# Optimization experiments

Hardware: AMD Instinct MI355X
Metric: run time of the kernel (lower is better)

Reference implementation:

```python
import jax, jax.numpy as jnp
import numpy as np

EPS_NORM = 1e-12   # F.normalize eps
EPS_DIST = 1e-4    # sqrt stabilizer from original code
EPSILON = 1e-8     # log stabilizer (forward default arg)


def setup_inputs() -> dict:
    key = jax.random.key(0)
    thought_vectors = jax.random.normal(key, (4, 2048, 1024), dtype=jnp.float32)
    return {"thought_vectors": thought_vectors}


def reference(thought_vectors):
    # NOTE: original code casts to fp32 then discards it by re-reshaping the
    # raw input; inputs here are already fp32 so the math is identical.
    D = thought_vectors.shape[-1]
    x = thought_vectors.reshape(-1, D)                          # [N, D]
    norm = jnp.linalg.norm(x, axis=-1, keepdims=True)
    x = x / jnp.maximum(norm, EPS_NORM)                         # L2 normalize
    N = x.shape[0]
    sim = jnp.minimum(jnp.einsum('nd,md->nm', x, x), 1.0)       # [N, N], clamp max=1
    dists = jnp.sqrt(2.0 - 2.0 * sim + EPS_DIST)                # chordal distance
    dists = jnp.where(jnp.eye(N, dtype=bool), jnp.inf, dists)   # mask self
    min_dist = jnp.min(dists, axis=1)                           # nearest neighbor
    return -jnp.mean(jnp.log(min_dist + EPSILON))
```

## Files before the change

### kernel.cpp

```cpp
#include <hip/hip_runtime.h>
#include <hip/hip_bf16.h>
#include <math.h>

#define N_ROWS 8192
#define DIM    1024
#define NB     (N_ROWS / 128)
#define NT     (NB * (NB + 1) / 2)

typedef __bf16 bf16_t;
typedef __bf16 bf16x4 __attribute__((ext_vector_type(4)));
typedef __bf16 bf16x8 __attribute__((ext_vector_type(8)));
typedef float  f32x4  __attribute__((ext_vector_type(4)));

#define GLOAD_LDS(g, s) __builtin_amdgcn_global_load_lds(                      \
    (const __attribute__((address_space(1))) void*)(g),                        \
    (__attribute__((address_space(3))) void*)(s), 16, 0, 0)

__device__ __forceinline__ unsigned fmap(float f) {
    unsigned u = __float_as_uint(f);
    return (u & 0x80000000u) ? ~u : (u | 0x80000000u);
}
__device__ __forceinline__ float funmap(unsigned u) {
    return (u & 0x80000000u) ? __uint_as_float(u ^ 0x80000000u)
                             : __uint_as_float(~u);
}

__global__ __launch_bounds__(256) void k_normalize(const float* __restrict__ x,
                                                   bf16_t* __restrict__ xb,
                                                   unsigned* __restrict__ row_max) {
    const int tid = threadIdx.x;
    const int l   = tid & 63;
    const int row = blockIdx.x * 4 + (tid >> 6);
    const float4* xr = reinterpret_cast<const float4*>(x + (size_t)row * DIM);

    float4 v[4];
    float ss = 0.0f;
    #pragma unroll
    for (int c = 0; c < 4; ++c) {
        v[c] = xr[l + c * 64];
        ss += v[c].x * v[c].x + v[c].y * v[c].y + v[c].z * v[c].z + v[c].w * v[c].w;
    }
    #pragma unroll
    for (int m = 32; m >= 1; m >>= 1) ss += __shfl_xor(ss, m);
    const float scale = 1.0f / fmaxf(sqrtf(ss), 1e-12f);

    bf16x4* xo = reinterpret_cast<bf16x4*>(xb + (size_t)row * DIM);
    #pragma unroll
    for (int c = 0; c < 4; ++c) {
        bf16x4 o;
        o[0] = (bf16_t)(v[c].x * scale);
        o[1] = (bf16_t)(v[c].y * scale);
        o[2] = (bf16_t)(v[c].z * scale);
        o[3] = (bf16_t)(v[c].w * scale);
        xo[l + c * 64] = o;
    }

    if (blockIdx.x < N_ROWS / 256)
        row_max[blockIdx.x * 256 + tid] = 0u;
}

__global__ __launch_bounds__(256) void k_simmax(const bf16_t* __restrict__ xb,
                                                unsigned* __restrict__ row_max) {
    __shared__ bf16_t smA[2][128 * 32];
    __shared__ bf16_t smB[2][128 * 32];
    const int tid = threadIdx.x;
    const int w  = tid >> 6;
    const int l  = tid & 63;
    const int lr = l & 15;
    const int lk = (l >> 4) * 8;
    const int wr = w >> 1, wc = w & 1;

    int t = blockIdx.x;
    #define TOFF(b) ((b) * NB - ((b) * ((b) - 1)) / 2)
    int bi = (int)((float)(2 * NB + 1 -
                sqrtf((float)((2 * NB + 1) * (2 * NB + 1) - 8 * t))) * 0.5f);
    if (bi < 0) bi = 0;
    if (bi > NB - 1) bi = NB - 1;
    while (TOFF(bi + 1) <= t) ++bi;
    while (TOFF(bi) > t) --bi;
    const int bj = bi + (t - TOFF(bi));
    const int i0 = bi * 128, j0 = bj * 128;

    const bf16_t* gA = xb + (size_t)(i0 + (tid >> 2)) * DIM + (tid & 3) * 8;
    const bf16_t* gB = xb + (size_t)(j0 + (tid >> 2)) * DIM + (tid & 3) * 8;
    const int wbase = (tid & ~63) * 8;

    #define STAGE(buf, kk) do {                                                \
        GLOAD_LDS(gA + (kk),            &smA[buf][wbase]);                     \
        GLOAD_LDS(gA + 64 * DIM + (kk), &smA[buf][2048 + wbase]);              \
        GLOAD_LDS(gB + (kk),            &smB[buf][wbase]);                     \
        GLOAD_LDS(gB + 64 * DIM + (kk), &smB[buf][2048 + wbase]);              \
    } while (0)

    f32x4 acc[4][4] = {};
    const int fa = (wr * 64 + lr) * 32 + lk;
    const int fb = (wc * 64 + lr) * 32 + lk;

    STAGE(0, 0);
    __syncthreads();
    int cur = 0;
    for (int k = 32; k < DIM; k += 32) {
        STAGE(cur ^ 1, k);
        bf16x8 af[4], bfr[4];
        #pragma unroll
        for (int m = 0; m < 4; ++m) af[m]  = *(const bf16x8*)(&smA[cur][fa + m * 512]);
        #pragma unroll
        for (int n = 0; n < 4; ++n) bfr[n] = *(const bf16x8*)(&smB[cur][fb + n * 512]);
        #pragma unroll
        for (int m = 0; m < 4; ++m)
            #pragma unroll
            for (int n = 0; n < 4; ++n)
                acc[m][n] = __builtin_amdgcn_mfma_f32_16x16x32_bf16(
                                af[m], bfr[n], acc[m][n], 0, 0, 0);
        __syncthreads();
        cur ^= 1;
    }
    {
        bf16x8 af[4], bfr[4];
        #pragma unroll
        for (int m = 0; m < 4; ++m) af[m]  = *(const bf16x8*)(&smA[cur][fa + m * 512]);
        #pragma unroll
        for (int n = 0; n < 4; ++n) bfr[n] = *(const bf16x8*)(&smB[cur][fb + n * 512]);
        #pragma unroll
        for (int m = 0; m < 4; ++m)
            #pragma unroll
            for (int n = 0; n < 4; ++n)
                acc[m][n] = __builtin_amdgcn_mfma_f32_16x16x32_bf16(
                                af[m], bfr[n], acc[m][n], 0, 0, 0);
    }

    #pragma unroll
    for (int m = 0; m < 4; ++m) {
        #pragma unroll
        for (int j = 0; j < 4; ++j) {
            const int rowg = i0 + wr * 64 + m * 16 + (l >> 4) * 4 + j;
            float rm = -3.0e38f;
            #pragma unroll
            for (int n = 0; n < 4; ++n) {
                float s = acc[m][n][j];
                if (rowg == (j0 + wc * 64 + n * 16 + lr)) s = -3.0e38f;
                rm = fmaxf(rm, s);
            }
            #pragma unroll
            for (int mask = 1; mask < 16; mask <<= 1)
                rm = fmaxf(rm, __shfl_xor(rm, mask));
            if (lr == 0)
                atomicMax(&row_max[rowg], fmap(fminf(rm, 1.0f)));
        }
    }
    if (bi != bj) {
        #pragma unroll
        for (int n = 0; n < 4; ++n) {
            const int colg = j0 + wc * 64 + n * 16 + lr;
            float cm = -3.0e38f;
            #pragma unroll
            for (int m = 0; m < 4; ++m)
                #pragma unroll
                for (int j = 0; j < 4; ++j)
                    cm = fmaxf(cm, acc[m][n][j]);
            cm = fmaxf(cm, __shfl_xor(cm, 16));
            cm = fmaxf(cm, __shfl_xor(cm, 32));
            if (l < 16)
                atomicMax(&row_max[colg], fmap(fminf(cm, 1.0f)));
        }
    }
}

__global__ __launch_bounds__(1024) void k_finish(const unsigned* __restrict__ row_max,
                                                 float* __restrict__ out) {
    const int tid = threadIdx.x;
    float sum = 0.0f;
    #pragma unroll
    for (int i = tid; i < N_ROWS; i += 1024) {
        float sim = fminf(funmap(row_max[i]), 1.0f);
        float dist = sqrtf(2.0f - 2.0f * sim + 1e-4f);
        sum += logf(dist + 1e-8f);
    }
    #pragma unroll
    for (int m = 32; m >= 1; m >>= 1) sum += __shfl_xor(sum, m);
    __shared__ float wss[16];
    if ((tid & 63) == 0) wss[tid >> 6] = sum;
    __syncthreads();
    if (tid == 0) {
        float tot = 0.0f;
        #pragma unroll
        for (int i = 0; i < 16; ++i) tot += wss[i];
        out[0] = -tot / (float)N_ROWS;
    }
}

extern "C" void kernel_launch(void* const* d_in, const int* in_sizes, int n_in,
                              void* d_out, int out_size, void* d_ws, size_t ws_size,
                              hipStream_t stream) {
    const float* x = (const float*)d_in[0];
    bf16_t* xb = (bf16_t*)d_ws;
    unsigned* row_max = (unsigned*)((char*)d_ws +
                         (size_t)N_ROWS * DIM * sizeof(bf16_t));
    float* out = (float*)d_out;

    k_normalize<<<N_ROWS / 4, 256, 0, stream>>>(x, xb, row_max);
    k_simmax<<<NT, 256, 0, stream>>>(xb, row_max);
    k_finish<<<1, 1024, 0, stream>>>(row_max, out);
}
```

Measured before the change: 191.5 us.

## Replace double-buffered K=32 staging with single-buffer K=64 tiles in simmax

The Gram-matrix kernel's K step grows from 32 to 64 per LDS stage, and the double buffer that overlapped the next tile's global-to-LDS load with MFMA work is dropped. Each iteration now loads a 128x64 tile of A and of B, synchronizes, runs two MFMA sub-steps, then synchronizes again. This halves the number of loop iterations and barriers. In exchange, load latency is no longer hidden behind compute within a block, so the kernel depends on other resident blocks to cover it. The row stride of 64 bf16 elements may also cause LDS bank conflicts on the fragment reads.

```diff
diff --git a/kernel.cpp b/kernel.cpp
--- a/kernel.cpp
+++ b/kernel.cpp
@@ -61,8 +61,8 @@
 
 __global__ __launch_bounds__(256) void k_simmax(const bf16_t* __restrict__ xb,
                                                 unsigned* __restrict__ row_max) {
-    __shared__ bf16_t smA[2][128 * 32];
-    __shared__ bf16_t smB[2][128 * 32];
+    __shared__ bf16_t smA[128 * 64];
+    __shared__ bf16_t smB[128 * 64];
     const int tid = threadIdx.x;
     const int w  = tid >> 6;
     const int l  = tid & 63;
@@ -81,52 +81,40 @@
     const int bj = bi + (t - TOFF(bi));
     const int i0 = bi * 128, j0 = bj * 128;
 
-    const bf16_t* gA = xb + (size_t)(i0 + (tid >> 2)) * DIM + (tid & 3) * 8;
-    const bf16_t* gB = xb + (size_t)(j0 + (tid >> 2)) * DIM + (tid & 3) * 8;
+    const int srow = tid >> 3, schk = (tid & 7) * 8;
+    const bf16_t* gA = xb + (size_t)(i0 + srow) * DIM + schk;
+    const bf16_t* gB = xb + (size_t)(j0 + srow) * DIM + schk;
     const int wbase = (tid & ~63) * 8;
 
-    #define STAGE(buf, kk) do {                                                \
-        GLOAD_LDS(gA + (kk),            &smA[buf][wbase]);                     \
-        GLOAD_LDS(gA + 64 * DIM + (kk), &smA[buf][2048 + wbase]);              \
-        GLOAD_LDS(gB + (kk),            &smB[buf][wbase]);                     \
-        GLOAD_LDS(gB + 64 * DIM + (kk), &smB[buf][2048 + wbase]);              \
-    } while (0)
+    f32x4 acc[4][4] = {};
+    const bf16_t* pa = smA + (wr * 64 + lr) * 64 + lk;
+    const bf16_t* pb = smB + (wc * 64 + lr) * 64 + lk;
 
-    f32x4 acc[4][4] = {};
-    const int fa = (wr * 64 + lr) * 32 + lk;
-    const int fb = (wc * 64 + lr) * 32 + lk;
+    for (int k = 0; k < DIM; k += 64) {
+        #pragma unroll
+        for (int q = 0; q < 4; ++q) {
+            GLOAD_LDS(gA + (size_t)(q * 32) * DIM + k, smA + q * 2048 + wbase);
+            GLOAD_LDS(gB + (size_t)(q * 32) * DIM + k, smB + q * 2048 + wbase);
+        }
+        __syncthreads();
 
-    STAGE(0, 0);
-    __syncthreads();
-    int cur = 0;
-    for (int k = 32; k < DIM; k += 32) {
-        STAGE(cur ^ 1, k);
-        bf16x8 af[4], bfr[4];
         #pragma unroll
-        for (int m = 0; m < 4; ++m) af[m]  = *(const bf16x8*)(&smA[cur][fa + m * 512]);
-        #pragma unroll
-        for (int n = 0; n < 4; ++n) bfr[n] = *(const bf16x8*)(&smB[cur][fb + n * 512]);
-        #pragma unroll
-        for (int m = 0; m < 4; ++m)
+        for (int ks = 0; ks < 2; ++ks) {
+            bf16x8 af[4], bfr[4];
+            #pragma unroll
+            for (int m = 0; m < 4; ++m)
+                af[m]  = *(const bf16x8*)(pa + m * 1024 + ks * 32);
             #pragma unroll
             for (int n = 0; n < 4; ++n)
-                acc[m][n] = __builtin_amdgcn_mfma_f32_16x16x32_bf16(
-                                af[m], bfr[n], acc[m][n], 0, 0, 0);
+                bfr[n] = *(const bf16x8*)(pb + n * 1024 + ks * 32);
+            #pragma unroll
+            for (int m = 0; m < 4; ++m)
+                #pragma unroll
+                for (int n = 0; n < 4; ++n)
+                    acc[m][n] = __builtin_amdgcn_mfma_f32_16x16x32_bf16(
+                                    af[m], bfr[n], acc[m][n], 0, 0, 0);
+        }
         __syncthreads();
-        cur ^= 1;
-    }
-    {
-        bf16x8 af[4], bfr[4];
-        #pragma unroll
-        for (int m = 0; m < 4; ++m) af[m]  = *(const bf16x8*)(&smA[cur][fa + m * 512]);
-        #pragma unroll
-        for (int n = 0; n < 4; ++n) bfr[n] = *(const bf16x8*)(&smB[cur][fb + n * 512]);
-        #pragma unroll
-        for (int m = 0; m < 4; ++m)
-            #pragma unroll
-            for (int n = 0; n < 4; ++n)
-                acc[m][n] = __builtin_amdgcn_mfma_f32_16x16x32_bf16(
-                                af[m], bfr[n], acc[m][n], 0, 0, 0);
     }
 
     #pragma unroll
```

Measured after the change: 210.9 us. 10.2% more time.
